# Kernel optimization log

Hardware: AMD Instinct MI355X
Metric: run time of the kernel (lower is better)

The kernel has to match this reference:

```python
import jax, jax.numpy as jnp
import numpy as np

B, N, E, H = 8, 16, 256, 256
EPS = 1e-5


def _ln(x, g, b):
    m = jnp.mean(x, axis=-1, keepdims=True)
    v = jnp.mean(jnp.square(x - m), axis=-1, keepdims=True)
    return (x - m) * jax.lax.rsqrt(v + EPS) * g + b


def setup_inputs() -> dict:
    key = jax.random.key(0)
    ks = jax.random.split(key, 24)
    s = 0.05
    inp = {
        "source_entities": jax.random.normal(ks[0], (B, N, E), jnp.float32),
        "source_relations": jax.random.uniform(ks[1], (B, N, N), jnp.float32),
        "target_entities": jax.random.normal(ks[2], (B, N, E), jnp.float32),
        "target_relations": jax.random.uniform(ks[3], (B, N, N), jnp.float32),
        # relation_encoder: Linear(2E->H), LayerNorm(H), ReLU, Linear(H->H)
        "rel_W1": jax.random.normal(ks[4], (2 * E, H), jnp.float32) * s,
        "rel_b1": jnp.zeros((H,), jnp.float32),
        "rel_g1": jnp.ones((H,), jnp.float32),
        "rel_be1": jnp.zeros((H,), jnp.float32),
        "rel_W2": jax.random.normal(ks[5], (H, H), jnp.float32) * s,
        "rel_b2": jnp.zeros((H,), jnp.float32),
        # mapping_network: Linear(2H->H), LayerNorm(H), ReLU, Linear(H->1)
        "map_W1": jax.random.normal(ks[6], (2 * H, H), jnp.float32) * s,
        "map_b1": jnp.zeros((H,), jnp.float32),
        "map_g": jnp.ones((H,), jnp.float32),
        "map_be": jnp.zeros((H,), jnp.float32),
        "map_W2": jax.random.normal(ks[7], (H, 1), jnp.float32) * s,
        "map_b2": jnp.zeros((1,), jnp.float32),
        # correspondence_scorer: Linear(2E->H), ReLU, Linear(H->1)
        "cor_W1": jax.random.normal(ks[8], (2 * E, H), jnp.float32) * s,
        "cor_b1": jnp.zeros((H,), jnp.float32),
        "cor_W2": jax.random.normal(ks[9], (H, 1), jnp.float32) * s,
        "cor_b2": jnp.zeros((1,), jnp.float32),
    }
    return inp


def _encode_relations(ent, rel, W1, b1, g1, be1, W2, b2):
    # ent: [B,N,E]; rel: [B,N,N].  Equivalent to cat([e_i, e_j]) @ W1 by
    # splitting W1 into the rows multiplying e_i and e_j (avoids concat).
    Wi, Wj = W1[:E], W1[E:]
    h = (jnp.einsum("bie,eh->bih", ent, Wi)[:, :, None, :]
         + jnp.einsum("bje,eh->bjh", ent, Wj)[:, None, :, :] + b1)  # [B,N,N,H]
    h = jax.nn.relu(_ln(h, g1, be1))
    h = jnp.einsum("bijh,hk->bijk", h, W2) + b2
    mask = (rel > 0).astype(h.dtype)[..., None]
    h = h * mask  # zeros where no relation, matching scatter into zeros tensor
    return h.reshape(ent.shape[0], N * N, H)


def _pairwise_score(a, b, W1, b1, W2, b2, g=None, be=None):
    # score over all (i,j) pairs: cat([a_i, b_j]) -> MLP -> scalar
    d = a.shape[-1]
    Wa, Wb = W1[:d], W1[d:]
    h = (jnp.einsum("bsd,dh->bsh", a, Wa)[:, :, None, :]
         + jnp.einsum("btd,dh->bth", b, Wb)[:, None, :, :] + b1)  # [B,S,T,H]
    if g is not None:
        h = _ln(h, g, be)
    h = jax.nn.relu(h)
    return (jnp.einsum("bsth,ho->bsto", h, W2) + b2)[..., 0]  # [B,S,T]


def reference(source_entities, source_relations, target_entities, target_relations,
              rel_W1, rel_b1, rel_g1, rel_be1, rel_W2, rel_b2,
              map_W1, map_b1, map_g, map_be, map_W2, map_b2,
              cor_W1, cor_b1, cor_W2, cor_b2):
    src_rel = _encode_relations(source_entities, source_relations,
                                rel_W1, rel_b1, rel_g1, rel_be1, rel_W2, rel_b2)
    tgt_rel = _encode_relations(target_entities, target_relations,
                                rel_W1, rel_b1, rel_g1, rel_be1, rel_W2, rel_b2)
    mapping_scores = _pairwise_score(src_rel, tgt_rel, map_W1, map_b1,
                                     map_W2, map_b2, map_g, map_be)
    corr_scores = _pairwise_score(source_entities, target_entities,
                                  cor_W1, cor_b1, cor_W2, cor_b2)
    mapping_scores = jax.nn.softmax(mapping_scores, axis=-1)
    corr_scores = jax.nn.softmax(corr_scores, axis=-1)
    return mapping_scores, corr_scores
```

## Files before the change

kernel.cpp:

```cpp
#include <hip/hip_runtime.h>

#define EDIM 256
#define HDIM 256

typedef float v2f __attribute__((ext_vector_type(2)));
__device__ __forceinline__ v2f splat2(float x) { v2f r; r.x = x; r.y = x; return r; }
__device__ __forceinline__ v2f mk2(float a, float b) { v2f r; r.x = a; r.y = b; return r; }
__device__ __forceinline__ v2f pkfma(v2f a, v2f b, v2f c) { return __builtin_elementwise_fma(a, b, c); }

__device__ __forceinline__ float waveAllSum(float v) {
  #pragma unroll
  for (int m = 32; m >= 1; m >>= 1) v += __shfl_xor(v, m, 64);
  return v;
}

__global__ __launch_bounds__(256) void k_proj(
    const float* __restrict__ srcE, const float* __restrict__ tgtE,
    const float* __restrict__ relW1, const float* __restrict__ relb1,
    const float* __restrict__ corW1, const float* __restrict__ corb1,
    const float* __restrict__ relW2, const float* __restrict__ relb2,
    const float* __restrict__ mapW1,
    float* __restrict__ Ps, float* __restrict__ Qs,
    float* __restrict__ Pt, float* __restrict__ Qt,
    float* __restrict__ CA, float* __restrict__ CB,
    float* __restrict__ Ca, float* __restrict__ Cb,
    float* __restrict__ da, float* __restrict__ db)
{
  const int which = blockIdx.x & 7;
  const int xb    = blockIdx.x >> 3;
  const int h     = threadIdx.x;
  if (which < 6 && xb >= 16) return;
  const int row0  = xb * 8;

  const float* A = nullptr; const float* W; const float* bias = nullptr;
  float* out;
  if (which == 0)      { A = srcE; W = relW1;              bias = relb1; out = Ps; }
  else if (which == 1) { A = srcE; W = relW1 + EDIM*HDIM;  out = Qs; }
  else if (which == 2) { A = tgtE; W = relW1;              bias = relb1; out = Pt; }
  else if (which == 3) { A = tgtE; W = relW1 + EDIM*HDIM;  out = Qt; }
  else if (which == 4) { A = srcE; W = corW1;              out = CA; }
  else if (which == 5) { A = tgtE; W = corW1 + EDIM*HDIM;  bias = corb1; out = CB; }
  else if (which == 6) { W = mapW1;                        out = Ca; }
  else                 { W = mapW1 + EDIM*HDIM;            out = Cb; }

  __shared__ float arow[8][EDIM];
  if (which < 6) {
    #pragma unroll
    for (int r = 0; r < 8; ++r) arow[r][h] = A[(row0 + r)*EDIM + h];
  } else if (xb < 32) {
    #pragma unroll
    for (int r = 0; r < 8; ++r) arow[r][h] = relW2[(row0 + r)*EDIM + h];
  } else {
    #pragma unroll
    for (int r = 0; r < 8; ++r) arow[r][h] = relb2[h];
  }
  __syncthreads();

  float acc[8];
  const float init = bias ? bias[h] : 0.0f;
  #pragma unroll
  for (int r = 0; r < 8; ++r) acc[r] = init;

  for (int d = 0; d < EDIM; d += 4) {
    const float w0 = W[(d+0)*HDIM + h];
    const float w1 = W[(d+1)*HDIM + h];
    const float w2 = W[(d+2)*HDIM + h];
    const float w3 = W[(d+3)*HDIM + h];
    #pragma unroll
    for (int r = 0; r < 8; ++r) {
      const float4 av = *(const float4*)&arow[r][d];
      acc[r] = fmaf(av.x,w0, fmaf(av.y,w1, fmaf(av.z,w2, fmaf(av.w,w3, acc[r]))));
    }
  }

  if (which < 6 || xb < 32) {
    #pragma unroll
    for (int r = 0; r < 8; ++r) out[(row0 + r)*HDIM + h] = acc[r];
  } else {
    float* d = (which == 6) ? da : db;
    d[h] = acc[0];
  }
}

__global__ __launch_bounds__(512) void k_encode(
    const float* __restrict__ Ps, const float* __restrict__ Qs,
    const float* __restrict__ relS,
    const float* __restrict__ Pt, const float* __restrict__ Qt,
    const float* __restrict__ relT,
    const float* __restrict__ g1, const float* __restrict__ be1,
    const float* __restrict__ Ca, const float* __restrict__ Cb,
    const float* __restrict__ da, const float* __restrict__ db,
    const float* __restrict__ mapb1,
    const float* __restrict__ mapg, const float* __restrict__ mapbe,
    const float* __restrict__ mapW2,
    float2* __restrict__ SAp, float* __restrict__ SAr, float* __restrict__ TB,
    float* __restrict__ rsS, float* __restrict__ qsS,
    float* __restrict__ rsT, float* __restrict__ qsT,
    float4* __restrict__ gbw)
{
  const int side = blockIdx.x & 1;
  const int bx   = blockIdx.x >> 1;
  const float* P   = side ? Pt   : Ps;
  const float* Q   = side ? Qt   : Qs;
  const float* rel = side ? relT : relS;

  const int row0 = bx * 8;
  const int b   = row0 >> 8;
  const int ij0 = row0 & 255;
  const int i   = ij0 >> 4;
  const int j0  = ij0 & 15;
  const int tid  = threadIdx.x;
  const int h    = tid & 255;
  const int rg   = tid >> 8;
  const int wave = tid >> 6;
  const int lane = tid & 63;

  if (side == 0 && bx == 0 && rg == 0)
    gbw[h] = make_float4(mapg[h], mapbe[h], mapW2[h], 0.0f);

  __shared__ v2f rlp[2][2][HDIM];
  __shared__ float red[8][8];

  const float pv = P[(b*16 + i)*HDIM + h];
  float x[4];
  #pragma unroll
  for (int r = 0; r < 4; ++r) x[r] = pv + Q[(b*16 + j0 + rg*4 + r)*HDIM + h];

  {
    float s1[4], s2[4];
    #pragma unroll
    for (int r = 0; r < 4; ++r) { s1[r] = x[r]; s2[r] = x[r]*x[r]; }
    #pragma unroll
    for (int m = 32; m >= 1; m >>= 1) {
      #pragma unroll
      for (int r = 0; r < 4; ++r) {
        s1[r] += __shfl_xor(s1[r], m, 64);
        s2[r] += __shfl_xor(s2[r], m, 64);
      }
    }
    if (lane == 0) {
      #pragma unroll
      for (int r = 0; r < 4; ++r) { red[wave][2*r] = s1[r]; red[wave][2*r+1] = s2[r]; }
    }
  }
  __syncthreads();

  {
    const float gh = g1[h], beh = be1[h];
    const int wb = rg*4;
    float val[4];
    #pragma unroll
    for (int r = 0; r < 4; ++r) {
      const float S1 = red[wb+0][2*r] + red[wb+1][2*r] + red[wb+2][2*r] + red[wb+3][2*r];
      const float S2 = red[wb+0][2*r+1] + red[wb+1][2*r+1] + red[wb+2][2*r+1] + red[wb+3][2*r+1];
      const float mean = S1 * (1.0f/256.0f);
      const float var  = S2 * (1.0f/256.0f) - mean*mean;
      const float rinv = rsqrtf(var + 1e-5f);
      val[r] = fmaxf(fmaf((x[r] - mean)*rinv, gh, beh), 0.0f);
    }
    rlp[rg][0][h] = mk2(val[0], val[1]);
    rlp[rg][1][h] = mk2(val[2], val[3]);
  }
  __syncthreads();

  const float* C = side ? Cb : Ca;
  v2f c01 = {0.f,0.f}, c23 = {0.f,0.f};
  #pragma unroll 2
  for (int k = 0; k < HDIM; k += 4) {
    const float w0 = C[(k+0)*HDIM + h];
    const float w1 = C[(k+1)*HDIM + h];
    const float w2 = C[(k+2)*HDIM + h];
    const float w3 = C[(k+3)*HDIM + h];
    const float4 pa = *(const float4*)&rlp[rg][0][k];
    const float4 pb = *(const float4*)&rlp[rg][0][k+2];
    const float4 qa = *(const float4*)&rlp[rg][1][k];
    const float4 qb = *(const float4*)&rlp[rg][1][k+2];
    c01 = pkfma(mk2(pa.x,pa.y), splat2(w0), c01);
    c01 = pkfma(mk2(pa.z,pa.w), splat2(w1), c01);
    c01 = pkfma(mk2(pb.x,pb.y), splat2(w2), c01);
    c01 = pkfma(mk2(pb.z,pb.w), splat2(w3), c01);
    c23 = pkfma(mk2(qa.x,qa.y), splat2(w0), c23);
    c23 = pkfma(mk2(qa.z,qa.w), splat2(w1), c23);
    c23 = pkfma(mk2(qb.x,qb.y), splat2(w2), c23);
    c23 = pkfma(mk2(qb.z,qb.w), splat2(w3), c23);
  }

  {
    const float dv = (side ? db : da)[h];
    c01 = c01 + splat2(dv);
    c23 = c23 + splat2(dv);
    const float* relRow = rel + (b*16 + i)*16;
    const int jb = j0 + rg*4;
    const v2f m01 = mk2(relRow[jb+0] > 0.f ? 1.f : 0.f, relRow[jb+1] > 0.f ? 1.f : 0.f);
    const v2f m23 = mk2(relRow[jb+2] > 0.f ? 1.f : 0.f, relRow[jb+3] > 0.f ? 1.f : 0.f);
    c01 = c01 * m01;
    c23 = c23 * m23;
    if (side) {
      const float mb = mapb1[h];
      c01 = c01 + splat2(mb);
      c23 = c23 + splat2(mb);
    }
  }

  {
    float s1[4] = {c01.x, c01.y, c23.x, c23.y};
    float s2[4] = {c01.x*c01.x, c01.y*c01.y, c23.x*c23.x, c23.y*c23.y};
    #pragma unroll
    for (int m = 32; m >= 1; m >>= 1) {
      #pragma unroll
      for (int r = 0; r < 4; ++r) {
        s1[r] += __shfl_xor(s1[r], m, 64);
        s2[r] += __shfl_xor(s2[r], m, 64);
      }
    }
    __syncthreads();
    if (lane == 0) {
      #pragma unroll
      for (int r = 0; r < 4; ++r) { red[wave][2*r] = s1[r]; red[wave][2*r+1] = s2[r]; }
    }
  }
  __syncthreads();
  if (tid < 16) {
    const int rg2 = tid >> 3, idx = tid & 7, r = idx >> 1;
    const int wb = rg2*4;
    const float v = red[wb+0][idx] + red[wb+1][idx] + red[wb+2][idx] + red[wb+3][idx];
    float* rs = side ? rsT : rsS;
    float* qs = side ? qsT : qsS;
    const int row = row0 + rg2*4 + r;
    if (idx & 1) qs[row] = v; else rs[row] = v;
  }

  const int rbase = row0 + rg*4;
  if (side == 0) {
    const int spBase = b*128 + ((ij0 + rg*4) >> 1);
    SAp[(spBase + 0)*HDIM + h] = make_float2(c01.x, c01.y);
    SAp[(spBase + 1)*HDIM + h] = make_float2(c23.x, c23.y);
    SAr[(rbase + 0)*HDIM + h] = c01.x;
    SAr[(rbase + 1)*HDIM + h] = c01.y;
    SAr[(rbase + 2)*HDIM + h] = c23.x;
    SAr[(rbase + 3)*HDIM + h] = c23.y;
  } else {
    TB[(rbase + 0)*HDIM + h] = c01.x;
    TB[(rbase + 1)*HDIM + h] = c01.y;
    TB[(rbase + 2)*HDIM + h] = c23.x;
    TB[(rbase + 3)*HDIM + h] = c23.y;
  }
}

__global__ __launch_bounds__(256) void k_cross(
    const float* __restrict__ SAr, const float* __restrict__ TB,
    float* __restrict__ G)
{
  const int b    = blockIdx.x & 7;
  const int rest = blockIdx.x >> 3;
  const int s0 = (rest & 7) * 32;
  const int t0 = (rest >> 3) * 32;
  const int tx = threadIdx.x & 15;
  const int ty = threadIdx.x >> 4;

  const float* SAb = SAr + ((b<<8) + s0)*HDIM;
  const float* TBb = TB  + ((b<<8) + t0)*HDIM;

  __shared__ float As[32][68], Bs[32][68];
  float acc00 = 0.f, acc01 = 0.f, acc10 = 0.f, acc11 = 0.f;

  const int lr = threadIdx.x >> 3;
  const int lc = (threadIdx.x & 7) * 8;

  for (int kk = 0; kk < HDIM; kk += 64) {
    *(float4*)&As[lr][lc]   = *(const float4*)&SAb[lr*HDIM + kk + lc];
    *(float4*)&As[lr][lc+4] = *(const float4*)&SAb[lr*HDIM + kk + lc + 4];
    *(float4*)&Bs[lr][lc]   = *(const float4*)&TBb[lr*HDIM + kk + lc];
    *(float4*)&Bs[lr][lc+4] = *(const float4*)&TBb[lr*HDIM + kk + lc + 4];
    __syncthreads();
    #pragma unroll
    for (int k = 0; k < 64; k += 4) {
      const float4 a0 = *(const float4*)&As[tx][k];
      const float4 a1 = *(const float4*)&As[tx+16][k];
      const float4 b0 = *(const float4*)&Bs[ty][k];
      const float4 b1 = *(const float4*)&Bs[ty+16][k];
      acc00 = fmaf(a0.x,b0.x, fmaf(a0.y,b0.y, fmaf(a0.z,b0.z, fmaf(a0.w,b0.w, acc00))));
      acc01 = fmaf(a0.x,b1.x, fmaf(a0.y,b1.y, fmaf(a0.z,b1.z, fmaf(a0.w,b1.w, acc01))));
      acc10 = fmaf(a1.x,b0.x, fmaf(a1.y,b0.y, fmaf(a1.z,b0.z, fmaf(a1.w,b0.w, acc10))));
      acc11 = fmaf(a1.x,b1.x, fmaf(a1.y,b1.y, fmaf(a1.z,b1.z, fmaf(a1.w,b1.w, acc11))));
    }
    __syncthreads();
  }

  float* Gb = G + (((b<<8) + t0)<<8) + s0;
  Gb[(ty   )*256 + tx     ] = acc00;
  Gb[(ty   )*256 + tx + 16] = acc10;
  Gb[(ty+16)*256 + tx     ] = acc01;
  Gb[(ty+16)*256 + tx + 16] = acc11;
}

__global__ __launch_bounds__(512) void k_scores(
    const float2* __restrict__ SApf, const float* __restrict__ TB,
    const float* __restrict__ G,
    const float* __restrict__ rsS, const float* __restrict__ qsS,
    const float* __restrict__ rsT, const float* __restrict__ qsT,
    const float4* __restrict__ gbw,
    const float* __restrict__ CA, const float* __restrict__ CB,
    const float* __restrict__ cW2,
    float* __restrict__ mapOut, float* __restrict__ corOut)
{
  const int wave = threadIdx.x >> 6;
  const int lane = threadIdx.x & 63;

  if (blockIdx.x >= 512) {
    const int bs = (blockIdx.x - 512)*8 + wave;
    const int b  = bs >> 4;
    const float4 ca4 = *(const float4*)(CA + bs*HDIM + lane*4);
    const float4 w24 = *(const float4*)(cW2 + lane*4);
    float sc[16];
    #pragma unroll
    for (int t = 0; t < 16; ++t) {
      const float4 cb4 = *(const float4*)(CB + (b*16 + t)*HDIM + lane*4);
      float p = fmaxf(ca4.x + cb4.x, 0.0f)*w24.x
              + fmaxf(ca4.y + cb4.y, 0.0f)*w24.y
              + fmaxf(ca4.z + cb4.z, 0.0f)*w24.z
              + fmaxf(ca4.w + cb4.w, 0.0f)*w24.w;
      sc[t] = waveAllSum(p);
    }
    float mx = sc[0];
    #pragma unroll
    for (int t = 1; t < 16; ++t) mx = fmaxf(mx, sc[t]);
    float se = 0.0f;
    #pragma unroll
    for (int t = 0; t < 16; ++t) { sc[t] = __expf(sc[t] - mx); se += sc[t]; }
    if (lane < 16) corOut[bs*16 + lane] = sc[lane] / se;
    return;
  }

  const int b  = blockIdx.x & 7;
  const int s0 = (blockIdx.x >> 3) * 4;
  const int tq = wave & 3;
  const int hw = wave >> 2;
  const int t  = (tq << 6) + lane;
  const int h0 = __builtin_amdgcn_readfirstlane(hw * 128);

  const float* tbrow = TB + ((b<<8) + t)*HDIM;
  const v2f* sp0 = (const v2f*)SApf + ((b<<7) + (s0>>1))*HDIM;
  const v2f* sp1 = sp0 + HDIM;

  v2f al01, bt01, al23, bt23;
  {
    const float4 gv = *(const float4*)&G[(((b<<8) + t)<<8) + s0];
    const float rt = rsT[(b<<8) + t];
    const float qt = qsT[(b<<8) + t];
    const float Gv[4] = {gv.x, gv.y, gv.z, gv.w};
    float alv[4], btv[4];
    #pragma unroll
    for (int si = 0; si < 4; ++si) {
      const float mean = (rsS[(b<<8) + s0 + si] + rt) * (1.0f/256.0f);
      const float e2   = (qsS[(b<<8) + s0 + si] + qt + 2.0f*Gv[si]) * (1.0f/256.0f);
      const float rinv = rsqrtf(e2 - mean*mean + 1e-5f);
      alv[si] = rinv;
      btv[si] = -mean * rinv;
    }
    al01 = mk2(alv[0], alv[1]); bt01 = mk2(btv[0], btv[1]);
    al23 = mk2(alv[2], alv[3]); bt23 = mk2(btv[2], btv[3]);
  }

  v2f acc01 = {0.f,0.f}, acc23 = {0.f,0.f};
  const v2f zero = {0.f,0.f};
  #pragma unroll 2
  for (int h = h0; h < h0 + 128; h += 4) {
    const float4 tb4 = *(const float4*)&tbrow[h];
    const v2f a0 = sp0[h], a1 = sp0[h+1], a2 = sp0[h+2], a3 = sp0[h+3];
    const v2f c0 = sp1[h], c1 = sp1[h+1], c2 = sp1[h+2], c3 = sp1[h+3];
    const float4 q0 = gbw[h], q1 = gbw[h+1], q2 = gbw[h+2], q3 = gbw[h+3];
    v2f u, r;
    u = pkfma(a0 + splat2(tb4.x), al01, bt01);
    r = __builtin_elementwise_max(pkfma(u, splat2(q0.x), splat2(q0.y)), zero);
    acc01 = pkfma(r, splat2(q0.z), acc01);
    u = pkfma(c0 + splat2(tb4.x), al23, bt23);
    r = __builtin_elementwise_max(pkfma(u, splat2(q0.x), splat2(q0.y)), zero);
    acc23 = pkfma(r, splat2(q0.z), acc23);

    u = pkfma(a1 + splat2(tb4.y), al01, bt01);
    r = __builtin_elementwise_max(pkfma(u, splat2(q1.x), splat2(q1.y)), zero);
    acc01 = pkfma(r, splat2(q1.z), acc01);
    u = pkfma(c1 + splat2(tb4.y), al23, bt23);
    r = __builtin_elementwise_max(pkfma(u, splat2(q1.x), splat2(q1.y)), zero);
    acc23 = pkfma(r, splat2(q1.z), acc23);

    u = pkfma(a2 + splat2(tb4.z), al01, bt01);
    r = __builtin_elementwise_max(pkfma(u, splat2(q2.x), splat2(q2.y)), zero);
    acc01 = pkfma(r, splat2(q2.z), acc01);
    u = pkfma(c2 + splat2(tb4.z), al23, bt23);
    r = __builtin_elementwise_max(pkfma(u, splat2(q2.x), splat2(q2.y)), zero);
    acc23 = pkfma(r, splat2(q2.z), acc23);

    u = pkfma(a3 + splat2(tb4.w), al01, bt01);
    r = __builtin_elementwise_max(pkfma(u, splat2(q3.x), splat2(q3.y)), zero);
    acc01 = pkfma(r, splat2(q3.z), acc01);
    u = pkfma(c3 + splat2(tb4.w), al23, bt23);
    r = __builtin_elementwise_max(pkfma(u, splat2(q3.x), splat2(q3.y)), zero);
    acc23 = pkfma(r, splat2(q3.z), acc23);
  }

  __shared__ float pg[2][4][4][64];
  pg[hw][tq][0][lane] = acc01.x;
  pg[hw][tq][1][lane] = acc01.y;
  pg[hw][tq][2][lane] = acc23.x;
  pg[hw][tq][3][lane] = acc23.y;
  __syncthreads();

  __shared__ float sc[4][256];
  if (hw == 0) {
    sc[0][t] = pg[0][tq][0][lane] + pg[1][tq][0][lane];
    sc[1][t] = pg[0][tq][1][lane] + pg[1][tq][1][lane];
    sc[2][t] = pg[0][tq][2][lane] + pg[1][tq][2][lane];
    sc[3][t] = pg[0][tq][3][lane] + pg[1][tq][3][lane];
  }
  __syncthreads();

  if (wave < 4) {
    float v0 = sc[wave][lane];
    float v1 = sc[wave][lane + 64];
    float v2 = sc[wave][lane + 128];
    float v3 = sc[wave][lane + 192];
    float mx = fmaxf(fmaxf(v0, v1), fmaxf(v2, v3));
    #pragma unroll
    for (int m = 32; m >= 1; m >>= 1) mx = fmaxf(mx, __shfl_xor(mx, m, 64));
    const float e0 = __expf(v0 - mx), e1 = __expf(v1 - mx);
    const float e2 = __expf(v2 - mx), e3 = __expf(v3 - mx);
    const float se = waveAllSum(e0 + e1 + e2 + e3);
    const float inv = 1.0f / se;
    float* orow = mapOut + ((b<<8) + s0 + wave)*256;
    orow[lane]       = e0 * inv;
    orow[lane + 64]  = e1 * inv;
    orow[lane + 128] = e2 * inv;
    orow[lane + 192] = e3 * inv;
  }
}

extern "C" void kernel_launch(void* const* d_in, const int* in_sizes, int n_in,
                              void* d_out, int out_size, void* d_ws, size_t ws_size,
                              hipStream_t stream) {
  const float* srcE  = (const float*)d_in[0];
  const float* srcR  = (const float*)d_in[1];
  const float* tgtE  = (const float*)d_in[2];
  const float* tgtR  = (const float*)d_in[3];
  const float* relW1 = (const float*)d_in[4];
  const float* relb1 = (const float*)d_in[5];
  const float* relg1 = (const float*)d_in[6];
  const float* relbe1= (const float*)d_in[7];
  const float* relW2 = (const float*)d_in[8];
  const float* relb2 = (const float*)d_in[9];
  const float* mapW1 = (const float*)d_in[10];
  const float* mapb1 = (const float*)d_in[11];
  const float* mapg  = (const float*)d_in[12];
  const float* mapbe = (const float*)d_in[13];
  const float* mapW2 = (const float*)d_in[14];
  const float* corW1 = (const float*)d_in[16];
  const float* corb1 = (const float*)d_in[17];
  const float* corW2 = (const float*)d_in[18];

  float* ws   = (float*)d_ws;
  float* Ps   = ws;
  float* Qs   = Ps   + 32768;
  float* Pt   = Qs   + 32768;
  float* Qt   = Pt   + 32768;
  float* CA   = Qt   + 32768;
  float* CB   = CA   + 32768;
  float2* SAp = (float2*)(CB + 32768);
  float* SAr  = (float*)(SAp + 262144);
  float* TB   = SAr + 524288;
  float* G    = TB  + 524288;
  float* rsS  = G + 524288;
  float* qsS  = rsS + 2048;
  float* rsT  = qsS + 2048;
  float* qsT  = rsT + 2048;
  float4* gbw = (float4*)(qsT + 2048);
  float* Ca   = (float*)gbw + 1024;
  float* Cb   = Ca + 65536;
  float* da   = Cb + 65536;
  float* db   = da + 256;

  float* mapOut = (float*)d_out;
  float* corOut = mapOut + 524288;

  k_proj<<<264, 256, 0, stream>>>(srcE, tgtE, relW1, relb1, corW1, corb1,
                                  relW2, relb2, mapW1,
                                  Ps, Qs, Pt, Qt, CA, CB,
                                  Ca, Cb, da, db);
  k_encode<<<512, 512, 0, stream>>>(Ps, Qs, srcR,
                                    Pt, Qt, tgtR,
                                    relg1, relbe1,
                                    Ca, Cb, da, db,
                                    mapb1, mapg, mapbe, mapW2,
                                    SAp, SAr, TB, rsS, qsS, rsT, qsT, gbw);
  k_cross<<<512, 256, 0, stream>>>(SAr, TB, G);
  k_scores<<<528, 512, 0, stream>>>(SAp, TB, G, rsS, qsS, rsT, qsT, gbw,
                                    CA, CB, corW2, mapOut, corOut);
}
```

Baseline: 67.14 us.

## Fuse cross-dot kernel into scoring kernel and transpose mapping weight layout

Removes the separate k_cross GEMM kernel and its SAr/G intermediates, and instead computes the source-target dot product G inside k_scores from the SAp and TB rows it already loads, reducing partial sums through shared memory. k_proj now writes the mapping-weight products transposed, so k_encode reads each thread's weight row with float4 loads instead of strided scalar loads. This cuts one kernel launch and a large intermediate write and read. The cost is extra FMA work and an additional barrier in k_scores, where the dot products are recomputed per block rather than shared through a tiled GEMM.

```diff
diff --git a/kernel.cpp b/kernel.cpp
--- a/kernel.cpp
+++ b/kernel.cpp
@@ -23,7 +23,7 @@
     float* __restrict__ Ps, float* __restrict__ Qs,
     float* __restrict__ Pt, float* __restrict__ Qt,
     float* __restrict__ CA, float* __restrict__ CB,
-    float* __restrict__ Ca, float* __restrict__ Cb,
+    float* __restrict__ Cat, float* __restrict__ Cbt,
     float* __restrict__ da, float* __restrict__ db)
 {
   const int which = blockIdx.x & 7;
@@ -40,8 +40,8 @@
   else if (which == 3) { A = tgtE; W = relW1 + EDIM*HDIM;  out = Qt; }
   else if (which == 4) { A = srcE; W = corW1;              out = CA; }
   else if (which == 5) { A = tgtE; W = corW1 + EDIM*HDIM;  bias = corb1; out = CB; }
-  else if (which == 6) { W = mapW1;                        out = Ca; }
-  else                 { W = mapW1 + EDIM*HDIM;            out = Cb; }
+  else if (which == 6) { W = mapW1;                        out = Cat; }
+  else                 { W = mapW1 + EDIM*HDIM;            out = Cbt; }
 
   __shared__ float arow[8][EDIM];
   if (which < 6) {
@@ -73,9 +73,17 @@
     }
   }
 
-  if (which < 6 || xb < 32) {
+  if (which < 6) {
     #pragma unroll
     for (int r = 0; r < 8; ++r) out[(row0 + r)*HDIM + h] = acc[r];
+  } else if (xb < 32) {
+    __syncthreads();
+    #pragma unroll
+    for (int r = 0; r < 8; ++r) arow[r][h] = acc[r];
+    __syncthreads();
+    float* o = out + (h<<8) + row0;
+    *(float4*)o       = make_float4(arow[0][h], arow[1][h], arow[2][h], arow[3][h]);
+    *(float4*)(o + 4) = make_float4(arow[4][h], arow[5][h], arow[6][h], arow[7][h]);
   } else {
     float* d = (which == 6) ? da : db;
     d[h] = acc[0];
@@ -88,12 +96,12 @@
     const float* __restrict__ Pt, const float* __restrict__ Qt,
     const float* __restrict__ relT,
     const float* __restrict__ g1, const float* __restrict__ be1,
-    const float* __restrict__ Ca, const float* __restrict__ Cb,
+    const float* __restrict__ Cat, const float* __restrict__ Cbt,
     const float* __restrict__ da, const float* __restrict__ db,
     const float* __restrict__ mapb1,
     const float* __restrict__ mapg, const float* __restrict__ mapbe,
     const float* __restrict__ mapW2,
-    float2* __restrict__ SAp, float* __restrict__ SAr, float* __restrict__ TB,
+    float2* __restrict__ SAp, float* __restrict__ TB,
     float* __restrict__ rsS, float* __restrict__ qsS,
     float* __restrict__ rsT, float* __restrict__ qsT,
     float4* __restrict__ gbw)
@@ -163,26 +171,23 @@
   }
   __syncthreads();
 
-  const float* C = side ? Cb : Ca;
+  const float4* crow = (const float4*)((side ? Cbt : Cat) + (h<<8));
   v2f c01 = {0.f,0.f}, c23 = {0.f,0.f};
   #pragma unroll 2
   for (int k = 0; k < HDIM; k += 4) {
-    const float w0 = C[(k+0)*HDIM + h];
-    const float w1 = C[(k+1)*HDIM + h];
-    const float w2 = C[(k+2)*HDIM + h];
-    const float w3 = C[(k+3)*HDIM + h];
+    const float4 cw = crow[k>>2];
     const float4 pa = *(const float4*)&rlp[rg][0][k];
     const float4 pb = *(const float4*)&rlp[rg][0][k+2];
     const float4 qa = *(const float4*)&rlp[rg][1][k];
     const float4 qb = *(const float4*)&rlp[rg][1][k+2];
-    c01 = pkfma(mk2(pa.x,pa.y), splat2(w0), c01);
-    c01 = pkfma(mk2(pa.z,pa.w), splat2(w1), c01);
-    c01 = pkfma(mk2(pb.x,pb.y), splat2(w2), c01);
-    c01 = pkfma(mk2(pb.z,pb.w), splat2(w3), c01);
-    c23 = pkfma(mk2(qa.x,qa.y), splat2(w0), c23);
-    c23 = pkfma(mk2(qa.z,qa.w), splat2(w1), c23);
-    c23 = pkfma(mk2(qb.x,qb.y), splat2(w2), c23);
-    c23 = pkfma(mk2(qb.z,qb.w), splat2(w3), c23);
+    c01 = pkfma(mk2(pa.x,pa.y), splat2(cw.x), c01);
+    c01 = pkfma(mk2(pa.z,pa.w), splat2(cw.y), c01);
+    c01 = pkfma(mk2(pb.x,pb.y), splat2(cw.z), c01);
+    c01 = pkfma(mk2(pb.z,pb.w), splat2(cw.w), c01);
+    c23 = pkfma(mk2(qa.x,qa.y), splat2(cw.x), c23);
+    c23 = pkfma(mk2(qa.z,qa.w), splat2(cw.y), c23);
+    c23 = pkfma(mk2(qb.x,qb.y), splat2(cw.z), c23);
+    c23 = pkfma(mk2(qb.z,qb.w), splat2(cw.w), c23);
   }
 
   {
@@ -235,10 +240,6 @@
     const int spBase = b*128 + ((ij0 + rg*4) >> 1);
     SAp[(spBase + 0)*HDIM + h] = make_float2(c01.x, c01.y);
     SAp[(spBase + 1)*HDIM + h] = make_float2(c23.x, c23.y);
-    SAr[(rbase + 0)*HDIM + h] = c01.x;
-    SAr[(rbase + 1)*HDIM + h] = c01.y;
-    SAr[(rbase + 2)*HDIM + h] = c23.x;
-    SAr[(rbase + 3)*HDIM + h] = c23.y;
   } else {
     TB[(rbase + 0)*HDIM + h] = c01.x;
     TB[(rbase + 1)*HDIM + h] = c01.y;
@@ -247,56 +248,8 @@
   }
 }
 
-__global__ __launch_bounds__(256) void k_cross(
-    const float* __restrict__ SAr, const float* __restrict__ TB,
-    float* __restrict__ G)
-{
-  const int b    = blockIdx.x & 7;
-  const int rest = blockIdx.x >> 3;
-  const int s0 = (rest & 7) * 32;
-  const int t0 = (rest >> 3) * 32;
-  const int tx = threadIdx.x & 15;
-  const int ty = threadIdx.x >> 4;
-
-  const float* SAb = SAr + ((b<<8) + s0)*HDIM;
-  const float* TBb = TB  + ((b<<8) + t0)*HDIM;
-
-  __shared__ float As[32][68], Bs[32][68];
-  float acc00 = 0.f, acc01 = 0.f, acc10 = 0.f, acc11 = 0.f;
-
-  const int lr = threadIdx.x >> 3;
-  const int lc = (threadIdx.x & 7) * 8;
-
-  for (int kk = 0; kk < HDIM; kk += 64) {
-    *(float4*)&As[lr][lc]   = *(const float4*)&SAb[lr*HDIM + kk + lc];
-    *(float4*)&As[lr][lc+4] = *(const float4*)&SAb[lr*HDIM + kk + lc + 4];
-    *(float4*)&Bs[lr][lc]   = *(const float4*)&TBb[lr*HDIM + kk + lc];
-    *(float4*)&Bs[lr][lc+4] = *(const float4*)&TBb[lr*HDIM + kk + lc + 4];
-    __syncthreads();
-    #pragma unroll
-    for (int k = 0; k < 64; k += 4) {
-      const float4 a0 = *(const float4*)&As[tx][k];
-      const float4 a1 = *(const float4*)&As[tx+16][k];
-      const float4 b0 = *(const float4*)&Bs[ty][k];
-      const float4 b1 = *(const float4*)&Bs[ty+16][k];
-      acc00 = fmaf(a0.x,b0.x, fmaf(a0.y,b0.y, fmaf(a0.z,b0.z, fmaf(a0.w,b0.w, acc00))));
-      acc01 = fmaf(a0.x,b1.x, fmaf(a0.y,b1.y, fmaf(a0.z,b1.z, fmaf(a0.w,b1.w, acc01))));
-      acc10 = fmaf(a1.x,b0.x, fmaf(a1.y,b0.y, fmaf(a1.z,b0.z, fmaf(a1.w,b0.w, acc10))));
-      acc11 = fmaf(a1.x,b1.x, fmaf(a1.y,b1.y, fmaf(a1.z,b1.z, fmaf(a1.w,b1.w, acc11))));
-    }
-    __syncthreads();
-  }
-
-  float* Gb = G + (((b<<8) + t0)<<8) + s0;
-  Gb[(ty   )*256 + tx     ] = acc00;
-  Gb[(ty   )*256 + tx + 16] = acc10;
-  Gb[(ty+16)*256 + tx     ] = acc01;
-  Gb[(ty+16)*256 + tx + 16] = acc11;
-}
-
 __global__ __launch_bounds__(512) void k_scores(
     const float2* __restrict__ SApf, const float* __restrict__ TB,
-    const float* __restrict__ G,
     const float* __restrict__ rsS, const float* __restrict__ qsS,
     const float* __restrict__ rsT, const float* __restrict__ qsT,
     const float4* __restrict__ gbw,
@@ -343,17 +296,35 @@
   const v2f* sp0 = (const v2f*)SApf + ((b<<7) + (s0>>1))*HDIM;
   const v2f* sp1 = sp0 + HDIM;
 
+  __shared__ float pg[2][4][4][64];
+
+  {
+    v2f G01 = {0.f,0.f}, G23 = {0.f,0.f};
+    #pragma unroll 2
+    for (int h = h0; h < h0 + 128; h += 4) {
+      const float4 tb4 = *(const float4*)&tbrow[h];
+      G01 = pkfma(sp0[h],   splat2(tb4.x), G01); G23 = pkfma(sp1[h],   splat2(tb4.x), G23);
+      G01 = pkfma(sp0[h+1], splat2(tb4.y), G01); G23 = pkfma(sp1[h+1], splat2(tb4.y), G23);
+      G01 = pkfma(sp0[h+2], splat2(tb4.z), G01); G23 = pkfma(sp1[h+2], splat2(tb4.z), G23);
+      G01 = pkfma(sp0[h+3], splat2(tb4.w), G01); G23 = pkfma(sp1[h+3], splat2(tb4.w), G23);
+    }
+    pg[hw][tq][0][lane] = G01.x;
+    pg[hw][tq][1][lane] = G01.y;
+    pg[hw][tq][2][lane] = G23.x;
+    pg[hw][tq][3][lane] = G23.y;
+  }
+  __syncthreads();
+
   v2f al01, bt01, al23, bt23;
   {
-    const float4 gv = *(const float4*)&G[(((b<<8) + t)<<8) + s0];
     const float rt = rsT[(b<<8) + t];
     const float qt = qsT[(b<<8) + t];
-    const float Gv[4] = {gv.x, gv.y, gv.z, gv.w};
     float alv[4], btv[4];
     #pragma unroll
     for (int si = 0; si < 4; ++si) {
+      const float Gf = pg[0][tq][si][lane] + pg[1][tq][si][lane];
       const float mean = (rsS[(b<<8) + s0 + si] + rt) * (1.0f/256.0f);
-      const float e2   = (qsS[(b<<8) + s0 + si] + qt + 2.0f*Gv[si]) * (1.0f/256.0f);
+      const float e2   = (qsS[(b<<8) + s0 + si] + qt + 2.0f*Gf) * (1.0f/256.0f);
       const float rinv = rsqrtf(e2 - mean*mean + 1e-5f);
       alv[si] = rinv;
       btv[si] = -mean * rinv;
@@ -361,6 +332,7 @@
     al01 = mk2(alv[0], alv[1]); bt01 = mk2(btv[0], btv[1]);
     al23 = mk2(alv[2], alv[3]); bt23 = mk2(btv[2], btv[3]);
   }
+  __syncthreads();
 
   v2f acc01 = {0.f,0.f}, acc23 = {0.f,0.f};
   const v2f zero = {0.f,0.f};
@@ -400,7 +372,6 @@
     acc23 = pkfma(r, splat2(q3.z), acc23);
   }
 
-  __shared__ float pg[2][4][4][64];
   pg[hw][tq][0][lane] = acc01.x;
   pg[hw][tq][1][lane] = acc01.y;
   pg[hw][tq][2][lane] = acc23.x;
@@ -466,17 +437,15 @@
   float* CA   = Qt   + 32768;
   float* CB   = CA   + 32768;
   float2* SAp = (float2*)(CB + 32768);
-  float* SAr  = (float*)(SAp + 262144);
-  float* TB   = SAr + 524288;
-  float* G    = TB  + 524288;
-  float* rsS  = G + 524288;
+  float* TB   = (float*)(SAp + 262144);
+  float* rsS  = TB + 524288;
   float* qsS  = rsS + 2048;
   float* rsT  = qsS + 2048;
   float* qsT  = rsT + 2048;
   float4* gbw = (float4*)(qsT + 2048);
-  float* Ca   = (float*)gbw + 1024;
-  float* Cb   = Ca + 65536;
-  float* da   = Cb + 65536;
+  float* Cat  = (float*)gbw + 1024;
+  float* Cbt  = Cat + 65536;
+  float* da   = Cbt + 65536;
   float* db   = da + 256;
 
   float* mapOut = (float*)d_out;
@@ -485,14 +454,13 @@
   k_proj<<<264, 256, 0, stream>>>(srcE, tgtE, relW1, relb1, corW1, corb1,
                                   relW2, relb2, mapW1,
                                   Ps, Qs, Pt, Qt, CA, CB,
-                                  Ca, Cb, da, db);
+                                  Cat, Cbt, da, db);
   k_encode<<<512, 512, 0, stream>>>(Ps, Qs, srcR,
                                     Pt, Qt, tgtR,
                                     relg1, relbe1,
-                                    Ca, Cb, da, db,
+                                    Cat, Cbt, da, db,
                                     mapb1, mapg, mapbe, mapW2,
-                                    SAp, SAr, TB, rsS, qsS, rsT, qsT, gbw);
-  k_cross<<<512, 256, 0, stream>>>(SAr, TB, G);
-  k_scores<<<528, 512, 0, stream>>>(SAp, TB, G, rsS, qsS, rsT, qsT, gbw,
+                                    SAp, TB, rsS, qsS, rsT, qsT, gbw);
+  k_scores<<<528, 512, 0, stream>>>(SAp, TB, rsS, qsS, rsT, qsT, gbw,
                                     CA, CB, corW2, mapOut, corOut);
 }
```

Result: slower. 88.65 us (+32.0%).
